# Kernel tuning notes

Hardware: AMD Instinct MI355X
Metric: run time of the kernel (lower is better)

## Reference

```python
import jax, jax.numpy as jnp
import numpy as np

B, T, C, F = 2, 2048, 2048, 8192
LN_EPS = 1e-5


def setup_inputs() -> dict:
    key = jax.random.key(0)
    ks = jax.random.split(key, 24)
    rn = lambda k, s, sc=1.0: jax.random.normal(k, s, jnp.float32) * sc
    un = lambda k, s: jax.random.uniform(k, s, jnp.float32)
    inp = {}
    inp['x'] = rn(ks[0], (B, T, C))
    inp['att_shift'] = rn(ks[1], (B, C))
    # wkv_state rows: aa (num), bb (den), pp (running max exponent)
    inp['wkv_state'] = jnp.stack([jnp.zeros((B, C)), jnp.zeros((B, C)),
                                  jnp.full((B, C), -1e38)], axis=1)
    inp['ffn_shift'] = rn(ks[2], (B, C))
    inp['ln1_g'] = jnp.ones(C); inp['ln1_b'] = jnp.zeros(C)
    inp['ln2_g'] = jnp.ones(C); inp['ln2_b'] = jnp.zeros(C)
    inp['tmk'] = un(ks[3], (C,)); inp['tmv'] = un(ks[4], (C,)); inp['tmr'] = un(ks[5], (C,))
    inp['time_decay'] = rn(ks[6], (C,), 0.5)
    inp['time_first'] = rn(ks[7], (C,), 0.5)
    inp['Wk'] = rn(ks[8], (C, C), 0.02); inp['Wv'] = rn(ks[9], (C, C), 0.02)
    inp['Wr'] = rn(ks[10], (C, C), 0.02); inp['Wo'] = rn(ks[11], (C, C), 0.02)
    inp['fmk'] = un(ks[12], (C,)); inp['fmr'] = un(ks[13], (C,))
    inp['Fk'] = rn(ks[14], (C, F), 0.02)
    inp['Fr'] = rn(ks[15], (C, C), 0.02)
    inp['Fv'] = rn(ks[16], (F, C), 0.02)
    return inp


def layer_norm(x, g, b):
    m = jnp.mean(x, axis=-1, keepdims=True)
    v = jnp.mean(jnp.square(x - m), axis=-1, keepdims=True)
    return (x - m) * jax.lax.rsqrt(v + LN_EPS) * g + b


def wkv(w, u, k, v, state):
    # w: -exp(time_decay) [C], u: time_first [C]; k,v: [B,T,C]; state: [B,3,C]
    def step(carry, kv_t):
        aa, bb, pp = carry
        kt, vt = kv_t
        ww = u + kt
        p = jnp.maximum(pp, ww)
        e1 = jnp.exp(pp - p)
        e2 = jnp.exp(ww - p)
        y = (e1 * aa + e2 * vt) / (e1 * bb + e2)
        ww2 = pp + w
        p2 = jnp.maximum(ww2, kt)
        e1b = jnp.exp(ww2 - p2)
        e2b = jnp.exp(kt - p2)
        return (e1b * aa + e2b * vt, e1b * bb + e2b, p2), y
    carry0 = (state[:, 0], state[:, 1], state[:, 2])
    (aa, bb, pp), ys = jax.lax.scan(step, carry0,
                                    (k.transpose(1, 0, 2), v.transpose(1, 0, 2)))
    return ys.transpose(1, 0, 2), jnp.stack([aa, bb, pp], axis=1)


def reference(x, att_shift, wkv_state, ffn_shift, ln1_g, ln1_b, ln2_g, ln2_b,
              tmk, tmv, tmr, time_decay, time_first, Wk, Wv, Wr, Wo,
              fmk, fmr, Fk, Fr, Fv):
    # ---- time-mix (attention) ----
    x1 = layer_norm(x, ln1_g, ln1_b)
    xx = jnp.concatenate([att_shift[:, None, :], x1[:, :-1]], axis=1)
    xk = x1 * tmk + xx * (1.0 - tmk)
    xv = x1 * tmv + xx * (1.0 - tmv)
    xr = x1 * tmr + xx * (1.0 - tmr)
    k = jnp.einsum('btc,cd->btd', xk, Wk)
    v = jnp.einsum('btc,cd->btd', xv, Wv)
    r = jnp.einsum('btc,cd->btd', xr, Wr)
    y, new_wkv = wkv(-jnp.exp(time_decay), time_first, k, v, wkv_state)
    x = x + jnp.einsum('btd,dc->btc', jax.nn.sigmoid(r) * y, Wo)
    # ---- channel-mix (FFN) ----
    x2 = layer_norm(x, ln2_g, ln2_b)
    xx2 = jnp.concatenate([ffn_shift[:, None, :], x2[:, :-1]], axis=1)
    xk2 = x2 * fmk + xx2 * (1.0 - fmk)
    xr2 = x2 * fmr + xx2 * (1.0 - fmr)
    kf = jnp.square(jax.nn.relu(jnp.einsum('btc,cf->btf', xk2, Fk)))
    kv = jnp.einsum('btf,fc->btc', kf, Fv)
    x = x + jax.nn.sigmoid(jnp.einsum('btc,cd->btd', xr2, Fr)) * kv
    return x, x1[:, -1], new_wkv, x2[:, -1]
```

## Files before the change

### kernel.cpp

```cpp
#include <hip/hip_runtime.h>
#include <stdint.h>

#define B_ 2
#define T_ 2048
#define C_ 2048
#define F_ 8192
#define M_ 4096
#define BC_ 4096
#define CHB 16
#define TCH 16
#define LC2 128

typedef __attribute__((ext_vector_type(8))) __bf16 bf16x8;
typedef __attribute__((ext_vector_type(4))) float f32x4;

__device__ __forceinline__ unsigned short f2bf(float f) {
  union { float f; unsigned u; } v; v.f = f;
  unsigned r = v.u + 0x7fffu + ((v.u >> 16) & 1u);
  return (unsigned short)(r >> 16);
}
__device__ __forceinline__ float b2f(unsigned short h) {
  union { unsigned u; float f; } v; v.u = ((unsigned)h) << 16; return v.f;
}

__device__ __forceinline__ void gload16(const void* g, void* l) {
  __builtin_amdgcn_global_load_lds((__attribute__((address_space(1))) void*)g,
                                   (__attribute__((address_space(3))) void*)l,
                                   16, 0, 0);
}

__global__ __launch_bounds__(256) void k_transpose_cast(
    const float* __restrict__ W, unsigned short* __restrict__ WT, int K, int N) {
  __shared__ unsigned short tile[32][33];
  const int n0 = blockIdx.x * 32, k0 = blockIdx.y * 32;
  const int tx = threadIdx.x & 31, ty = threadIdx.x >> 5;
#pragma unroll
  for (int i = 0; i < 4; ++i)
    tile[ty + 8 * i][tx] = f2bf(W[(size_t)(k0 + ty + 8 * i) * N + n0 + tx]);
  __syncthreads();
#pragma unroll
  for (int i = 0; i < 4; ++i)
    WT[(size_t)(n0 + ty + 8 * i) * K + k0 + tx] = tile[tx][ty + 8 * i];
}

__global__ __launch_bounds__(256) void k_layernorm(
    const float* __restrict__ x, const float* __restrict__ g,
    const float* __restrict__ beta, unsigned short* __restrict__ y,
    float* __restrict__ last_out) {
  const int row = blockIdx.x;
  const int t = row & (T_ - 1);
  const int bi = row >> 11;
  const float* xr = x + (size_t)row * C_;
  const int base = threadIdx.x * 8;
  float lv[8];
  {
    float4 a = *(const float4*)(xr + base);
    float4 b = *(const float4*)(xr + base + 4);
    lv[0]=a.x; lv[1]=a.y; lv[2]=a.z; lv[3]=a.w; lv[4]=b.x; lv[5]=b.y; lv[6]=b.z; lv[7]=b.w;
  }
  float s = 0.f, q = 0.f;
#pragma unroll
  for (int j = 0; j < 8; ++j) { s += lv[j]; q += lv[j] * lv[j]; }
#pragma unroll
  for (int o = 32; o > 0; o >>= 1) { s += __shfl_down(s, o); q += __shfl_down(q, o); }
  __shared__ float rs[4], rq[4];
  if ((threadIdx.x & 63) == 0) { rs[threadIdx.x >> 6] = s; rq[threadIdx.x >> 6] = q; }
  __syncthreads();
  s = rs[0] + rs[1] + rs[2] + rs[3];
  q = rq[0] + rq[1] + rq[2] + rq[3];
  const float mean = s * (1.f / C_);
  const float var = q * (1.f / C_) - mean * mean;
  const float inv = 1.f / sqrtf(var + 1e-5f);
  float ov[8];
  unsigned short o8[8];
#pragma unroll
  for (int j = 0; j < 8; ++j) {
    ov[j] = (lv[j] - mean) * inv * g[base + j] + beta[base + j];
    o8[j] = f2bf(ov[j]);
  }
  *(uint4*)(y + (size_t)row * C_ + base) = *(uint4*)o8;
  if (last_out != nullptr && t == T_ - 1) {
    float* lp = last_out + (size_t)bi * C_ + base;
    *(float4*)lp = make_float4(ov[0], ov[1], ov[2], ov[3]);
    *(float4*)(lp + 4) = make_float4(ov[4], ov[5], ov[6], ov[7]);
  }
}

__global__ __launch_bounds__(256) void k_mix3(
    const unsigned short* __restrict__ x1, const float* __restrict__ shift,
    const float* __restrict__ tmk, const float* __restrict__ tmv,
    const float* __restrict__ tmr,
    unsigned short* __restrict__ xk, unsigned short* __restrict__ xv,
    unsigned short* __restrict__ xr) {
  const int row = blockIdx.x;
  const int t = row & (T_ - 1);
  const int bi = row >> 11;
  const int c0 = threadIdx.x * 8;
  const size_t o = (size_t)row * C_ + c0;
  unsigned short cur8[8];
  *(uint4*)cur8 = *(const uint4*)(x1 + o);
  float pv[8];
  if (t == 0) {
    const float* sp = shift + (size_t)bi * C_ + c0;
#pragma unroll
    for (int j = 0; j < 8; ++j) pv[j] = sp[j];
  } else {
    unsigned short p8[8];
    *(uint4*)p8 = *(const uint4*)(x1 + o - C_);
#pragma unroll
    for (int j = 0; j < 8; ++j) pv[j] = b2f(p8[j]);
  }
  unsigned short ok[8], ov[8], orr[8];
#pragma unroll
  for (int j = 0; j < 8; ++j) {
    const float a = b2f(cur8[j]), p = pv[j];
    const float mk = tmk[c0 + j], mv = tmv[c0 + j], mr = tmr[c0 + j];
    ok[j]  = f2bf(a * mk + p * (1.f - mk));
    ov[j]  = f2bf(a * mv + p * (1.f - mv));
    orr[j] = f2bf(a * mr + p * (1.f - mr));
  }
  *(uint4*)(xk + o) = *(uint4*)ok;
  *(uint4*)(xv + o) = *(uint4*)ov;
  *(uint4*)(xr + o) = *(uint4*)orr;
}

__global__ __launch_bounds__(256) void k_mix2(
    const unsigned short* __restrict__ x2, const float* __restrict__ shift,
    const float* __restrict__ fmk, const float* __restrict__ fmr,
    unsigned short* __restrict__ xk2, unsigned short* __restrict__ xr2) {
  const int row = blockIdx.x;
  const int t = row & (T_ - 1);
  const int bi = row >> 11;
  const int c0 = threadIdx.x * 8;
  const size_t o = (size_t)row * C_ + c0;
  unsigned short cur8[8];
  *(uint4*)cur8 = *(const uint4*)(x2 + o);
  float pv[8];
  if (t == 0) {
    const float* sp = shift + (size_t)bi * C_ + c0;
#pragma unroll
    for (int j = 0; j < 8; ++j) pv[j] = sp[j];
  } else {
    unsigned short p8[8];
    *(uint4*)p8 = *(const uint4*)(x2 + o - C_);
#pragma unroll
    for (int j = 0; j < 8; ++j) pv[j] = b2f(p8[j]);
  }
  unsigned short ok[8], orr[8];
#pragma unroll
  for (int j = 0; j < 8; ++j) {
    const float a = b2f(cur8[j]), p = pv[j];
    const float mk = fmk[c0 + j], mr = fmr[c0 + j];
    ok[j]  = f2bf(a * mk + p * (1.f - mk));
    orr[j] = f2bf(a * mr + p * (1.f - mr));
  }
  *(uint4*)(xk2 + o) = *(uint4*)ok;
  *(uint4*)(xr2 + o) = *(uint4*)orr;
}

__global__ __launch_bounds__(256) void k_wkv_blk(
    const float* __restrict__ kk, const float* __restrict__ vv,
    const float* __restrict__ td, const float* __restrict__ tf,
    const float* __restrict__ st, float* __restrict__ y,
    float* __restrict__ out_state) {
  __shared__ float sA[TCH][CHB], sB[TCH][CHB], sP[TCH][CHB];
  const int blk = blockIdx.x;
  const int bi = blk >> 7;
  const int tx = threadIdx.x & 15;
  const int ty = threadIdx.x >> 4;
  const int c = ((blk & 127) * CHB) + tx;
  const float w = -expf(td[c]);
  const float u = tf[c];
  const size_t base = (size_t)bi * T_ * C_ + (size_t)ty * LC2 * C_ + c;
  const float* kp = kk + base;
  const float* vp = vv + base;
  float aa = 0.f, bb = 0.f, pp = -1e38f;
#pragma unroll 8
  for (int i = 0; i < LC2; ++i) {
    const float kt = kp[(size_t)i * C_], vt = vp[(size_t)i * C_];
    const float ww2 = pp + w;
    const float p2 = fmaxf(ww2, kt);
    const float e1b = expf(ww2 - p2), e2b = expf(kt - p2);
    aa = e1b * aa + e2b * vt;
    bb = e1b * bb + e2b;
    pp = p2;
  }
  sA[ty][tx] = aa; sB[ty][tx] = bb; sP[ty][tx] = pp;
  __syncthreads();
  if (ty == 0) {
    const float* s0 = st + (size_t)bi * 3 * C_;
    float ca = s0[c], cb = s0[C_ + c], cp = s0[2 * C_ + c];
    const float wL = w * (float)LC2;
#pragma unroll
    for (int j = 0; j < TCH; ++j) {
      const float a2 = sA[j][tx], b2 = sB[j][tx], p2 = sP[j][tx];
      sA[j][tx] = ca; sB[j][tx] = cb; sP[j][tx] = cp;
      const float pd = cp + wL;
      const float pm = fmaxf(pd, p2);
      const float e1 = expf(pd - pm), e2 = expf(p2 - pm);
      ca = e1 * ca + e2 * a2;
      cb = e1 * cb + e2 * b2;
      cp = pm;
    }
  }
  __syncthreads();
  aa = sA[ty][tx]; bb = sB[ty][tx]; pp = sP[ty][tx];
  float* yp = y + base;
#pragma unroll 4
  for (int i = 0; i < LC2; ++i) {
    const float kt = kp[(size_t)i * C_], vt = vp[(size_t)i * C_];
    const float ww = u + kt;
    const float p = fmaxf(pp, ww);
    const float e1 = expf(pp - p), e2 = expf(ww - p);
    yp[(size_t)i * C_] = (e1 * aa + e2 * vt) / (e1 * bb + e2);
    const float ww2 = pp + w;
    const float p2 = fmaxf(ww2, kt);
    const float e1b = expf(ww2 - p2), e2b = expf(kt - p2);
    aa = e1b * aa + e2b * vt;
    bb = e1b * bb + e2b;
    pp = p2;
  }
  if (ty == TCH - 1) {
    float* ob = out_state + (size_t)bi * 3 * C_;
    ob[c] = aa; ob[C_ + c] = bb; ob[2 * C_ + c] = pp;
  }
}

__global__ __launch_bounds__(256) void k_sry(
    const unsigned short* __restrict__ r, const float* __restrict__ y,
    unsigned short* __restrict__ sry) {
  const int nv = M_ * C_ / 8;
  for (int i = blockIdx.x * 256 + threadIdx.x; i < nv; i += gridDim.x * 256) {
    unsigned short r8[8];
    *(uint4*)r8 = ((const uint4*)r)[i];
    float4 ya = ((const float4*)y)[2 * i], yb = ((const float4*)y)[2 * i + 1];
    const float yv[8] = {ya.x, ya.y, ya.z, ya.w, yb.x, yb.y, yb.z, yb.w};
    unsigned short o8[8];
#pragma unroll
    for (int j = 0; j < 8; ++j) {
      const float s = 1.f / (1.f + expf(-b2f(r8[j])));
      o8[j] = f2bf(s * yv[j]);
    }
    ((uint4*)sry)[i] = *(uint4*)o8;
  }
}

template <int EPI, int SWZ>
__global__ __launch_bounds__(512, 1) void k_gemm8(
    const unsigned short* __restrict__ A, const unsigned short* __restrict__ BT,
    int K, int Nn, void* __restrict__ out,
    const float* __restrict__ aux1, const float* __restrict__ aux2) {
  __shared__ unsigned short lds[73728];
  const int tid = threadIdx.x;
  const int lane = tid & 63;
  const int wid = tid >> 6;
  int mBase, nBase;
  if (SWZ) {
    const int gx = gridDim.x;
    int wg = blockIdx.y * gx + blockIdx.x;
    const int nwg = gx * gridDim.y;
    wg = (wg & 7) * (nwg >> 3) + (wg >> 3);
    mBase = (wg / gx) * 128;
    nBase = (wg % gx) * 256;
  } else {
    mBase = blockIdx.y * 128;
    nBase = blockIdx.x * 256;
  }
  const int wr = (wid >> 2) * 64;
  const int wc = (wid & 3) * 64;
  const int r16 = lane & 15, kq = lane >> 4;
  const int lrow = lane >> 3;
  const int lslot = (lane & 7) ^ lrow;
  const int xsw = r16 & 7;
  f32x4 acc[4][4] = {};

  const unsigned short* gA0 = A  + (size_t)(mBase + 0   + wid * 8 + lrow) * K + lslot * 8;
  const unsigned short* gA1 = A  + (size_t)(mBase + 64  + wid * 8 + lrow) * K + lslot * 8;
  const unsigned short* gB0 = BT + (size_t)(nBase + 0   + wid * 8 + lrow) * K + lslot * 8;
  const unsigned short* gB1 = BT + (size_t)(nBase + 64  + wid * 8 + lrow) * K + lslot * 8;
  const unsigned short* gB2 = BT + (size_t)(nBase + 128 + wid * 8 + lrow) * K + lslot * 8;
  const unsigned short* gB3 = BT + (size_t)(nBase + 192 + wid * 8 + lrow) * K + lslot * 8;
  const int wof = wid * 512;

  const int nt = K >> 6;
  gload16(gA0, &lds[0 + wof]);
  gload16(gA1, &lds[4096 + wof]);
  gload16(gB0, &lds[8192 + wof]);
  gload16(gB1, &lds[12288 + wof]);
  gload16(gB2, &lds[16384 + wof]);
  gload16(gB3, &lds[20480 + wof]);
  gload16(gA0 + 64, &lds[24576 + 0 + wof]);
  gload16(gA1 + 64, &lds[24576 + 4096 + wof]);
  gload16(gB0 + 64, &lds[24576 + 8192 + wof]);
  gload16(gB1 + 64, &lds[24576 + 12288 + wof]);
  gload16(gB2 + 64, &lds[24576 + 16384 + wof]);
  gload16(gB3 + 64, &lds[24576 + 20480 + wof]);
  asm volatile("s_waitcnt vmcnt(6)" ::: "memory");
  asm volatile("s_barrier" ::: "memory");

  int cb = 0;
  for (int t = 0; t < nt; ++t) {
    const int nb = (cb >= 1) ? cb - 1 : 2;
    const int ca = cb * 24576;
    const int cbo = cb * 24576 + 8192;
    const int nba = nb * 24576;
    const int kb2 = (t + 2) << 6;
    const bool pf = (t + 2) < nt;
    bf16x8 af[2][2], bq[2][2];
#pragma unroll
    for (int qm = 0; qm < 2; ++qm) {
#pragma unroll
      for (int qn = 0; qn < 2; ++qn) {
        if (qn == 0) {
#pragma unroll
          for (int dm = 0; dm < 2; ++dm)
#pragma unroll
            for (int s = 0; s < 2; ++s)
              af[dm][s] = *(const bf16x8*)&lds[ca + (wr + (qm * 2 + dm) * 16 + r16) * 64 +
                                               (((s * 4 + kq) ^ xsw) * 8)];
        }
#pragma unroll
        for (int dn = 0; dn < 2; ++dn)
#pragma unroll
          for (int s = 0; s < 2; ++s)
            bq[dn][s] = *(const bf16x8*)&lds[cbo + (wc + (qn * 2 + dn) * 16 + r16) * 64 +
                                             (((s * 4 + kq) ^ xsw) * 8)];
        const int ph = qm * 2 + qn;
        if (pf) {
          if (ph == 0) {
            gload16(gA0 + kb2, &lds[nba + 0 + wof]);
            gload16(gA1 + kb2, &lds[nba + 4096 + wof]);
          } else if (ph == 1) {
            gload16(gB0 + kb2, &lds[nba + 8192 + wof]);
            gload16(gB1 + kb2, &lds[nba + 12288 + wof]);
          } else if (ph == 2) {
            gload16(gB2 + kb2, &lds[nba + 16384 + wof]);
            gload16(gB3 + kb2, &lds[nba + 20480 + wof]);
          }
        }
        asm volatile("s_barrier" ::: "memory");
        __builtin_amdgcn_s_setprio(1);
#pragma unroll
        for (int dm = 0; dm < 2; ++dm)
#pragma unroll
          for (int dn = 0; dn < 2; ++dn)
#pragma unroll
            for (int s = 0; s < 2; ++s)
              acc[qm * 2 + dm][qn * 2 + dn] = __builtin_amdgcn_mfma_f32_16x16x32_bf16(
                  af[dm][s], bq[dn][s], acc[qm * 2 + dm][qn * 2 + dn], 0, 0, 0);
        __builtin_amdgcn_s_setprio(0);
        if (ph == 3) {
          if (pf) {
            asm volatile("s_waitcnt vmcnt(6)" ::: "memory");
          } else if (t + 1 < nt) {
            asm volatile("s_waitcnt vmcnt(0)" ::: "memory");
          }
        }
        asm volatile("s_barrier" ::: "memory");
      }
    }
    cb = (cb == 2) ? 0 : cb + 1;
  }

  const int c0 = kq * 4;
#pragma unroll
  for (int m = 0; m < 4; ++m) {
#pragma unroll
    for (int n = 0; n < 4; ++n) {
      const int col = nBase + wc + n * 16 + r16;
#pragma unroll
      for (int e = 0; e < 4; ++e) {
        const int rowg = mBase + wr + m * 16 + c0 + e;
        const size_t idx = (size_t)rowg * Nn + col;
        const float va = acc[m][n][e];
        if (EPI == 0) {
          ((float*)out)[idx] = va;
        } else if (EPI == 1) {
          const float t = va > 0.f ? va : 0.f;
          ((unsigned short*)out)[idx] = f2bf(t * t);
        } else if (EPI == 2) {
          ((float*)out)[idx] = aux1[idx] + va;
        } else if (EPI == 3) {
          const float s = 1.f / (1.f + expf(-va));
          ((float*)out)[idx] = aux1[idx] + s * aux2[idx];
        } else {
          ((unsigned short*)out)[idx] = f2bf(va);
        }
      }
    }
  }
}

extern "C" void kernel_launch(void* const* d_in, const int* in_sizes, int n_in,
                              void* d_out, int out_size, void* d_ws, size_t ws_size,
                              hipStream_t stream) {
  const float* x          = (const float*)d_in[0];
  const float* att_shift  = (const float*)d_in[1];
  const float* wkv_state  = (const float*)d_in[2];
  const float* ffn_shift  = (const float*)d_in[3];
  const float* ln1_g = (const float*)d_in[4];
  const float* ln1_b = (const float*)d_in[5];
  const float* ln2_g = (const float*)d_in[6];
  const float* ln2_b = (const float*)d_in[7];
  const float* tmk = (const float*)d_in[8];
  const float* tmv = (const float*)d_in[9];
  const float* tmr = (const float*)d_in[10];
  const float* time_decay = (const float*)d_in[11];
  const float* time_first = (const float*)d_in[12];
  const float* Wk = (const float*)d_in[13];
  const float* Wv = (const float*)d_in[14];
  const float* Wr = (const float*)d_in[15];
  const float* Wo = (const float*)d_in[16];
  const float* fmk = (const float*)d_in[17];
  const float* fmr = (const float*)d_in[18];
  const float* Fk = (const float*)d_in[19];
  const float* Fr = (const float*)d_in[20];
  const float* Fv = (const float*)d_in[21];

  const size_t MB = 1ull << 20;
  char* ws = (char*)d_ws;
  if (ws_size < 176 * MB) return;

  unsigned short* Wslot = (unsigned short*)(ws);
  float*          kBuf  = (float*)(ws + 32 * MB);
  float*          vBuf  = (float*)(ws + 64 * MB);
  float*          yBuf  = (float*)(ws + 96 * MB);
  unsigned short* h1    = (unsigned short*)(ws + 128 * MB);
  unsigned short* h2    = (unsigned short*)(ws + 144 * MB);
  unsigned short* h3    = (unsigned short*)(ws + 160 * MB);
  unsigned short* xrT   = (unsigned short*)kBuf;
  unsigned short* kf    = (unsigned short*)kBuf;
  float*          kv    = (float*)h1;

  float* outb    = (float*)d_out;
  float* x1_last = outb + (size_t)M_ * C_;
  float* wkv_out = x1_last + (size_t)B_ * C_;
  float* x2_last = wkv_out + (size_t)B_ * 3 * C_;

  const dim3 gCC(C_ / 32, C_ / 32);
  const dim3 gC8(C_ / 256, M_ / 128);
  const dim3 gF8(F_ / 256, M_ / 128);

  k_layernorm<<<M_, 256, 0, stream>>>(x, ln1_g, ln1_b, h1, x1_last);
  k_mix3<<<M_, 256, 0, stream>>>(h1, att_shift, tmk, tmv, tmr, h2, h3, xrT);
  k_transpose_cast<<<gCC, 256, 0, stream>>>(Wr, Wslot, C_, C_);
  k_gemm8<4,0><<<gC8, 512, 0, stream>>>(xrT, Wslot, C_, C_, h1, nullptr, nullptr);
  k_transpose_cast<<<gCC, 256, 0, stream>>>(Wk, Wslot, C_, C_);
  k_gemm8<0,0><<<gC8, 512, 0, stream>>>(h2, Wslot, C_, C_, kBuf, nullptr, nullptr);
  k_transpose_cast<<<gCC, 256, 0, stream>>>(Wv, Wslot, C_, C_);
  k_gemm8<0,0><<<gC8, 512, 0, stream>>>(h3, Wslot, C_, C_, vBuf, nullptr, nullptr);
  k_wkv_blk<<<dim3(BC_ / CHB), 256, 0, stream>>>(kBuf, vBuf, time_decay, time_first,
                                                 wkv_state, yBuf, wkv_out);
  k_sry<<<1024, 256, 0, stream>>>(h1, yBuf, h2);
  k_transpose_cast<<<gCC, 256, 0, stream>>>(Wo, Wslot, C_, C_);
  k_gemm8<2,0><<<gC8, 512, 0, stream>>>(h2, Wslot, C_, C_, yBuf, x, nullptr);

  k_layernorm<<<M_, 256, 0, stream>>>(yBuf, ln2_g, ln2_b, h1, x2_last);
  k_mix2<<<M_, 256, 0, stream>>>(h1, ffn_shift, fmk, fmr, h2, h3);
  k_transpose_cast<<<dim3(F_ / 32, C_ / 32), 256, 0, stream>>>(Fk, Wslot, C_, F_);
  k_gemm8<1,1><<<gF8, 512, 0, stream>>>(h2, Wslot, C_, F_, kf, nullptr, nullptr);
  k_transpose_cast<<<dim3(C_ / 32, F_ / 32), 256, 0, stream>>>(Fv, Wslot, F_, C_);
  k_gemm8<0,1><<<gC8, 512, 0, stream>>>(kf, Wslot, F_, C_, kv, nullptr, nullptr);
  k_transpose_cast<<<gCC, 256, 0, stream>>>(Fr, Wslot, C_, C_);
  k_gemm8<3,0><<<gC8, 512, 0, stream>>>(h3, Wslot, C_, C_, d_out, yBuf, kv);
}
```

Measured before the change: 740.8 us.

## Collapse GEMM inner loop to one barrier per k-tile with bulk prefetch

Replaces the four-phase ping-pong schedule in the bf16 GEMM main loop, which interleaved partial LDS reads, staged global prefetches and two barriers per phase. Now each k-tile issues all six global prefetches at once, loads all A/B fragments from LDS, runs 32 MFMAs, and synchronises with a single barrier. LDS offsets are precomputed outside the loop to cut address arithmetic. This removes seven of the eight barriers per k-tile and simplifies scheduling. The cost is higher register pressure from holding 16 fragments, and less fine-grained interleaving of memory and compute across waves.

```diff
diff --git a/kernel.cpp b/kernel.cpp
--- a/kernel.cpp
+++ b/kernel.cpp
@@ -281,6 +281,17 @@
   const unsigned short* gB2 = BT + (size_t)(nBase + 128 + wid * 8 + lrow) * K + lslot * 8;
   const unsigned short* gB3 = BT + (size_t)(nBase + 192 + wid * 8 + lrow) * K + lslot * 8;
   const int wof = wid * 512;
+  int aoff[4][2], boff[4][2];
+#pragma unroll
+  for (int m = 0; m < 4; ++m)
+#pragma unroll
+    for (int s = 0; s < 2; ++s)
+      aoff[m][s] = (wr + m * 16 + r16) * 64 + (((s * 4 + kq) ^ xsw) * 8);
+#pragma unroll
+  for (int n = 0; n < 4; ++n)
+#pragma unroll
+    for (int s = 0; s < 2; ++s)
+      boff[n][s] = 8192 + (wc + n * 16 + r16) * 64 + (((s * 4 + kq) ^ xsw) * 8);
 
   const int nt = K >> 6;
   gload16(gA0, &lds[0 + wof]);
@@ -302,63 +313,44 @@
   for (int t = 0; t < nt; ++t) {
     const int nb = (cb >= 1) ? cb - 1 : 2;
     const int ca = cb * 24576;
-    const int cbo = cb * 24576 + 8192;
     const int nba = nb * 24576;
     const int kb2 = (t + 2) << 6;
     const bool pf = (t + 2) < nt;
-    bf16x8 af[2][2], bq[2][2];
-#pragma unroll
-    for (int qm = 0; qm < 2; ++qm) {
-#pragma unroll
-      for (int qn = 0; qn < 2; ++qn) {
-        if (qn == 0) {
-#pragma unroll
-          for (int dm = 0; dm < 2; ++dm)
-#pragma unroll
-            for (int s = 0; s < 2; ++s)
-              af[dm][s] = *(const bf16x8*)&lds[ca + (wr + (qm * 2 + dm) * 16 + r16) * 64 +
-                                               (((s * 4 + kq) ^ xsw) * 8)];
-        }
-#pragma unroll
-        for (int dn = 0; dn < 2; ++dn)
-#pragma unroll
-          for (int s = 0; s < 2; ++s)
-            bq[dn][s] = *(const bf16x8*)&lds[cbo + (wc + (qn * 2 + dn) * 16 + r16) * 64 +
-                                             (((s * 4 + kq) ^ xsw) * 8)];
-        const int ph = qm * 2 + qn;
-        if (pf) {
-          if (ph == 0) {
-            gload16(gA0 + kb2, &lds[nba + 0 + wof]);
-            gload16(gA1 + kb2, &lds[nba + 4096 + wof]);
-          } else if (ph == 1) {
-            gload16(gB0 + kb2, &lds[nba + 8192 + wof]);
-            gload16(gB1 + kb2, &lds[nba + 12288 + wof]);
-          } else if (ph == 2) {
-            gload16(gB2 + kb2, &lds[nba + 16384 + wof]);
-            gload16(gB3 + kb2, &lds[nba + 20480 + wof]);
-          }
-        }
-        asm volatile("s_barrier" ::: "memory");
-        __builtin_amdgcn_s_setprio(1);
-#pragma unroll
-        for (int dm = 0; dm < 2; ++dm)
-#pragma unroll
-          for (int dn = 0; dn < 2; ++dn)
-#pragma unroll
-            for (int s = 0; s < 2; ++s)
-              acc[qm * 2 + dm][qn * 2 + dn] = __builtin_amdgcn_mfma_f32_16x16x32_bf16(
-                  af[dm][s], bq[dn][s], acc[qm * 2 + dm][qn * 2 + dn], 0, 0, 0);
-        __builtin_amdgcn_s_setprio(0);
-        if (ph == 3) {
-          if (pf) {
-            asm volatile("s_waitcnt vmcnt(6)" ::: "memory");
-          } else if (t + 1 < nt) {
-            asm volatile("s_waitcnt vmcnt(0)" ::: "memory");
-          }
-        }
-        asm volatile("s_barrier" ::: "memory");
-      }
+    if (pf) {
+      gload16(gA0 + kb2, &lds[nba + 0 + wof]);
+      gload16(gA1 + kb2, &lds[nba + 4096 + wof]);
+      gload16(gB0 + kb2, &lds[nba + 8192 + wof]);
+      gload16(gB1 + kb2, &lds[nba + 12288 + wof]);
+      gload16(gB2 + kb2, &lds[nba + 16384 + wof]);
+      gload16(gB3 + kb2, &lds[nba + 20480 + wof]);
     }
+    bf16x8 af[4][2], bq[4][2];
+#pragma unroll
+    for (int m = 0; m < 4; ++m)
+#pragma unroll
+      for (int s = 0; s < 2; ++s)
+        af[m][s] = *(const bf16x8*)&lds[ca + aoff[m][s]];
+#pragma unroll
+    for (int n = 0; n < 4; ++n)
+#pragma unroll
+      for (int s = 0; s < 2; ++s)
+        bq[n][s] = *(const bf16x8*)&lds[ca + boff[n][s]];
+    __builtin_amdgcn_s_setprio(1);
+#pragma unroll
+    for (int m = 0; m < 4; ++m)
+#pragma unroll
+      for (int n = 0; n < 4; ++n)
+#pragma unroll
+        for (int s = 0; s < 2; ++s)
+          acc[m][n] = __builtin_amdgcn_mfma_f32_16x16x32_bf16(
+              af[m][s], bq[n][s], acc[m][n], 0, 0, 0);
+    __builtin_amdgcn_s_setprio(0);
+    if (pf) {
+      asm volatile("s_waitcnt vmcnt(6)" ::: "memory");
+    } else if (t + 1 < nt) {
+      asm volatile("s_waitcnt vmcnt(0)" ::: "memory");
+    }
+    asm volatile("s_barrier" ::: "memory");
     cb = (cb == 2) ? 0 : cb + 1;
   }
 
```

Result: faster. 695.5 us (-6.1%).
